# Optimization experiments

Measured on AMD Instinct MI355X. Metric: run time of the kernel, lower is better.

Reference implementation:

```python
import jax, jax.numpy as jnp
import numpy as np

MODEL_DIM = 128
N_FRAMES = 128
N_SAMPLES = 32768
N_TABLES = 8
TABLE_SIZE = 512
BATCH = 8
N_FREQS = 16


def _mlp(x, w1, b1, w2, b2, w3, b3):
    # LinearOutputStack(channels, 3, ...): Linear -> lrelu -> Linear -> lrelu -> Linear
    h = jax.nn.leaky_relu(x @ w1 + b1, 0.2)
    h = jax.nn.leaky_relu(h @ w2 + b2, 0.2)
    return h @ w3 + b3


def _pos_encoded(t, n_freqs=N_FREQS):
    # (t, 1 + 2*n_freqs) = (t, 33): raw position plus sin/cos at geometric freqs
    pos = jnp.linspace(-1.0, 1.0, t, dtype=jnp.float32)
    scales = (2.0 ** jnp.arange(n_freqs, dtype=jnp.float32)) * jnp.pi
    ang = pos[:, None] * scales[None, :]
    return jnp.concatenate([pos[:, None], jnp.sin(ang), jnp.cos(ang)], axis=-1)


def _interp_linear(env, out_size):
    # torch F.interpolate(mode='linear', align_corners=False) from (B, F) to (B, out_size)
    f = env.shape[-1]
    coord = (jnp.arange(out_size, dtype=jnp.float32) + 0.5) * (f / out_size) - 0.5
    i0 = jnp.floor(coord)
    frac = (coord - i0).astype(env.dtype)
    i0c = jnp.clip(i0, 0, f - 1).astype(jnp.int32)
    i1c = jnp.clip(i0 + 1, 0, f - 1).astype(jnp.int32)
    return env[:, i0c] * (1.0 - frac) + env[:, i1c] * frac


def setup_inputs() -> dict:
    key = jax.random.key(0)
    ks = jax.random.split(key, 16)
    wi = 0.02  # weight_init from Experiment
    d = MODEL_DIM

    def lin(k, i, o):
        return jax.random.normal(k, (i, o), jnp.float32) * wi

    inp = {
        "x": jax.random.normal(ks[0], (BATCH, d), jnp.float32),
        "wavetables": jax.random.uniform(ks[1], (N_TABLES, TABLE_SIZE), jnp.float32, -1.0, 1.0),
    }
    specs = {"tc": (d, N_TABLES), "env": (d, N_FRAMES), "pos": (33, d), "sk": (d, TABLE_SIZE)}
    i = 2
    for name, (cin, cout) in specs.items():
        k1, k2, k3 = jax.random.split(ks[i], 3)
        inp[f"{name}_w1"] = lin(k1, cin, d)
        inp[f"{name}_b1"] = jnp.zeros((d,), jnp.float32)
        inp[f"{name}_w2"] = lin(k2, d, d)
        inp[f"{name}_b2"] = jnp.zeros((d,), jnp.float32)
        inp[f"{name}_w3"] = lin(k3, d, cout)
        inp[f"{name}_b3"] = jnp.zeros((cout,), jnp.float32)
        i += 1
    return inp


def reference(x, wavetables,
              tc_w1, tc_b1, tc_w2, tc_b2, tc_w3, tc_b3,
              env_w1, env_b1, env_w2, env_b2, env_w3, env_b3,
              pos_w1, pos_b1, pos_w2, pos_b2, pos_w3, pos_b3,
              sk_w1, sk_b1, sk_w2, sk_b2, sk_w3, sk_b3):
    # table choice: softmax then hard max (straight value * gathered table)
    c = jax.nn.softmax(_mlp(x, tc_w1, tc_b1, tc_w2, tc_b2, tc_w3, tc_b3), axis=-1)
    values = jnp.max(c, axis=-1)          # (B,)
    indices = jnp.argmax(c, axis=-1)      # (B,)

    mx = jnp.max(wavetables, axis=-1, keepdims=True)
    wt = wavetables / (mx + 1e-8)
    sel = wt[indices]                     # (B, TABLE_SIZE)

    env = jnp.abs(_mlp(x, env_w1, env_b1, env_w2, env_b2, env_w3, env_b3))  # (B, N_FRAMES)
    env = _interp_linear(env, N_SAMPLES)  # (B, N_SAMPLES)

    # pos encoding is identical across batch; embed once then broadcast (same math)
    pe = _pos_encoded(N_SAMPLES)          # (T, 33)
    pos = _mlp(pe, pos_w1, pos_b1, pos_w2, pos_b2, pos_w3, pos_b3)  # (T, D)
    pos = pos[None, :, :] + x[:, None, :]  # (B, T, D)

    sk = jax.nn.softmax(_mlp(pos, sk_w1, sk_b1, sk_w2, sk_b2, sk_w3, sk_b3), axis=-1)  # (B, T, K)

    # selected_tables (B,1,K) @ kernel^T (B,K,T) -> (B,1,T)
    sampled = jnp.einsum('bk,btk->bt', sel, sk)
    sampled = sampled * env * values[:, None]
    return sampled[:, None, :]
```

## Files before the change

### kernel.cpp

```cpp
#include <hip/hip_runtime.h>
#include <math.h>

#define D 128
#define B 8
#define T_SAMP 32768
#define K 512
#define NT 8
#define NFRM 128

#define WS_C1   0
#define WS_ENV8 1024
#define WS_SEL  2048
#define WS_VAL  6144
#define WS_B3P  6160
#define WSBF_BYTE 32768
#define OP1 0
#define OP2 9216
#define OP3 26624
#define OS1 44032
#define OS2 61440
#define OS3 78848
#define WTOT 148480
#define WS_NEED (WSBF_BYTE + WTOT*2)

typedef __attribute__((ext_vector_type(8))) short short8;
typedef __attribute__((ext_vector_type(4))) float f32x4;

#define LOG2E 1.4426950408889634f

__device__ __forceinline__ float lrelu(float v){ return fmaxf(v, 0.2f*v); }

__device__ __forceinline__ unsigned cvtpk(float lo, float hi){
    unsigned r;
    asm("v_cvt_pk_bf16_f32 %0, %1, %2" : "=v"(r) : "v"(lo), "v"(hi));
    return r;
}
__device__ __forceinline__ unsigned short bfr(float f){
    unsigned u = __builtin_bit_cast(unsigned, f); u += 0x7fffu + ((u>>16)&1u);
    return (unsigned short)(u>>16);
}
__device__ __forceinline__ float bf2f(short s){
    unsigned u = ((unsigned)(unsigned short)s) << 16;
    return __builtin_bit_cast(float, u);
}
__device__ __forceinline__ float exp2fast(float x){
#if __has_builtin(__builtin_amdgcn_exp2f)
    return __builtin_amdgcn_exp2f(x);
#else
    return __expf(x*0.6931471805599453f);
#endif
}
__device__ __forceinline__ float sin_rev(float fr){
#if __has_builtin(__builtin_amdgcn_sinf)
    return __builtin_amdgcn_sinf(fr);
#else
    return __sinf(fr*6.283185307179586f);
#endif
}
__device__ __forceinline__ float cos_rev(float fr){
#if __has_builtin(__builtin_amdgcn_cosf)
    return __builtin_amdgcn_cosf(fr);
#else
    return __cosf(fr*6.283185307179586f);
#endif
}
__device__ __forceinline__ float pe_val(float pf, int j){
    if (j == 0) return pf;
    if (j > 32) return 0.f;
    const bool is_sin = (j <= 16);
    int e = is_sin ? (j + 125) : (j + 109);
    float sc = __builtin_bit_cast(float, ((unsigned)e) << 23);
    float u = pf * sc;
    float fr = u - floorf(u);
    return is_sin ? sin_rev(fr) : cos_rev(fr);
}

#define VMCNT0 asm volatile("s_waitcnt vmcnt(0)" ::: "memory")

__device__ void layer128(const float* __restrict__ in, const float* __restrict__ w,
                         const float* __restrict__ bias, float* __restrict__ outp,
                         int tid, int mode)
{
    int n = tid & 127, bg = tid >> 7;
    const float* i0 = in + (bg*4+0)*D;
    const float* i1 = in + (bg*4+1)*D;
    const float* i2 = in + (bg*4+2)*D;
    const float* i3 = in + (bg*4+3)*D;
    float bb = bias[n];
    float a0=bb,a1=bb,a2=bb,a3=bb;
    for (int j=0;j<D;j++){
        float wv = w[j*D+n];
        a0 = fmaf(i0[j], wv, a0);
        a1 = fmaf(i1[j], wv, a1);
        a2 = fmaf(i2[j], wv, a2);
        a3 = fmaf(i3[j], wv, a3);
    }
    if (mode==0){ a0=lrelu(a0);a1=lrelu(a1);a2=lrelu(a2);a3=lrelu(a3); }
    else if (mode==1){ a0=fabsf(a0);a1=fabsf(a1);a2=fabsf(a2);a3=fabsf(a3); }
    outp[(bg*4+0)*D+n]=a0;
    outp[(bg*4+1)*D+n]=a1;
    outp[(bg*4+2)*D+n]=a2;
    outp[(bg*4+3)*D+n]=a3;
}

__global__ __launch_bounds__(256) void setup_kernel(
    const float* __restrict__ x, const float* __restrict__ wt,
    const float* __restrict__ tc_w1, const float* __restrict__ tc_b1,
    const float* __restrict__ tc_w2, const float* __restrict__ tc_b2,
    const float* __restrict__ tc_w3, const float* __restrict__ tc_b3,
    const float* __restrict__ env_w1, const float* __restrict__ env_b1,
    const float* __restrict__ env_w2, const float* __restrict__ env_b2,
    const float* __restrict__ env_w3, const float* __restrict__ env_b3,
    const float* __restrict__ sk_w1, const float* __restrict__ sk_b1,
    const float* __restrict__ pos_w1, const float* __restrict__ pos_w2,
    const float* __restrict__ pos_w3, const float* __restrict__ sk_w2,
    const float* __restrict__ sk_w3, const float* __restrict__ sk_b3,
    float* __restrict__ ws)
{
    __shared__ float xl[B*D], buf1[B*D], buf2[B*D];
    __shared__ float lgts[B*NT], pmax[NT*8], mxr[NT];
    __shared__ int idxl[B];
    int tid = threadIdx.x;

    if (blockIdx.x != 0){
        int idx = (blockIdx.x - 1)*256 + tid;
        if (idx >= WTOT) return;
        unsigned short* wb = (unsigned short*)((char*)ws + WSBF_BYTE);
        float v;
        if (idx < OP2){
            int n = idx/72, k = idx%72;
            v = (k < 33) ? pos_w1[k*D + n] : 0.f;
        } else if (idx < OS3){
            int r = idx - OP2; int wsel = r/17408; int i = r%17408;
            int n = i/136, k = i%136;
            const float* W = wsel==0?pos_w2: wsel==1?pos_w3: wsel==2? sk_w1 : sk_w2;
            v = (k < 128) ? W[k*D + n] : 0.f;
        } else {
            int i = idx - OS3; int n = i/136, k = i%136;
            v = (k < 128) ? sk_w3[k*K + n] : 0.f;
        }
        wb[idx] = bfr(v);
        return;
    }

    for (int i=tid;i<B*D;i+=256) xl[i]=x[i];
    for (int i=tid;i<K;i+=256) ws[WS_B3P+i] = sk_b3[i]*LOG2E;
    __syncthreads();
    layer128(xl, tc_w1, tc_b1, buf1, tid, 0);
    __syncthreads();
    layer128(buf1, tc_w2, tc_b2, buf2, tid, 0);
    __syncthreads();
    if (tid < 64){
        int b = tid>>3, n = tid&7;
        float a = tc_b3[n];
        for (int j=0;j<D;j++) a = fmaf(buf2[b*D+j], tc_w3[j*NT+n], a);
        lgts[b*NT+n] = a;
    } else if (tid < 128){
        int r = (tid-64)>>3, p = tid&7;
        float m = -1e30f;
        for (int k=p*64;k<p*64+64;k++) m = fmaxf(m, wt[r*K+k]);
        pmax[r*8+p] = m;
    }
    __syncthreads();
    if (tid < 8){
        int b = tid; float m = -1e30f; int idx = 0;
        for (int n=0;n<NT;n++){ float v = lgts[b*NT+n]; if (v > m){ m=v; idx=n; } }
        float S = 0.f;
        for (int n=0;n<NT;n++) S += expf(lgts[b*NT+n]-m);
        ws[WS_VAL+b] = 1.0f/S;
        idxl[b] = idx;
    } else if (tid < 16){
        int r = tid-8; float m = -1e30f;
        for (int p=0;p<8;p++) m = fmaxf(m, pmax[r*8+p]);
        mxr[r] = m;
    }
    __syncthreads();
    for (int o=tid;o<B*K;o+=256){
        int b = o>>9, k = o&(K-1);
        int id = idxl[b];
        ws[WS_SEL+o] = wt[id*K+k] / (mxr[id] + 1e-8f);
    }
    layer128(xl, env_w1, env_b1, buf1, tid, 0);
    __syncthreads();
    layer128(buf1, env_w2, env_b2, buf2, tid, 0);
    __syncthreads();
    layer128(buf2, env_w3, env_b3, ws+WS_ENV8, tid, 1);
    layer128(xl, sk_w1, sk_b1, ws+WS_C1, tid, 2);
}

template<int NKT, int KSTR, bool ACT>
__device__ __forceinline__ void layerG(const unsigned char* Wp, const unsigned char* inb,
                                       unsigned char* outb, const float* biasp,
                                       int wv, int lg, int lc)
{
    const f32x4 z = {0.f,0.f,0.f,0.f};
    short8 aw[NKT];
    #pragma unroll
    for (int kt=0;kt<NKT;kt++)
        aw[kt] = *(const short8*)(Wp + ((16*wv+lc)*KSTR + 32*kt + 8*lg)*2);
    f32x4 bb = z;
    if (biasp) bb = *(const f32x4*)(biasp + 16*wv + 4*lg);
    #pragma unroll
    for (int rt=0;rt<2;rt++){
        f32x4 d = z;
        #pragma unroll
        for (int kt=0;kt<NKT;kt++){
            short8 bf = *(const short8*)(inb + ((16*rt+lc)*KSTR + 32*kt + 8*lg)*2);
            d = __builtin_amdgcn_mfma_f32_16x16x32_bf16(aw[kt], bf, d, 0,0,0);
        }
        float o0 = d[0]+bb[0], o1 = d[1]+bb[1], o2 = d[2]+bb[2], o3 = d[3]+bb[3];
        if (ACT){ o0=lrelu(o0); o1=lrelu(o1); o2=lrelu(o2); o3=lrelu(o3); }
        uint2 u; u.x = cvtpk(o0,o1); u.y = cvtpk(o2,o3);
        *(uint2*)(outb + ((16*rt+lc)*136 + 16*wv + 4*lg)*2) = u;
    }
}

__global__ __launch_bounds__(512, 4) void synth3(
    const float* __restrict__ pos_b1, const float* __restrict__ pos_b2,
    const float* __restrict__ pos_b3, const float* __restrict__ sk_b2,
    const float* __restrict__ ws, float* __restrict__ out)
{
    __shared__ __align__(16) unsigned char lds[52224];
    unsigned char* WREG_ = lds;
    unsigned char* abA   = lds + 34816;
    unsigned char* abB   = lds + 43520;
    unsigned char* PEb   = abB;

    const int tid = threadIdx.x;
    const int wv = tid >> 6, lane = tid & 63, lg = lane >> 4, lc = lane & 15;
    const int t0 = blockIdx.x * 32;
    const unsigned char* wg = (const unsigned char*)ws + WSBF_BYTE;
    const f32x4 z = {0.f,0.f,0.f,0.f};

    auto stage = [&](int elemoff, unsigned char* dst, int nchunks){
        const unsigned char* src = wg + (size_t)elemoff*2;
        for (int c = wv; c < nchunks; c += 8)
            __builtin_amdgcn_global_load_lds(
                (const __attribute__((address_space(1))) unsigned int*)(src + (c<<10) + lane*16),
                (__attribute__((address_space(3))) unsigned int*)(dst + (c<<10)), 16, 0, 0);
    };

    stage(OP1, WREG_, 18);
    for (int i = tid; i < 1152; i += 512){
        int r = i/36, j0 = (i - r*36)*2;
        float pf = (float)(-1.0 + 2.0*(double)(t0+r)/32767.0);
        float v0 = pe_val(pf, j0);
        float v1 = pe_val(pf, j0+1);
        *(unsigned*)(PEb + (r*72 + j0)*2) = cvtpk(v0, v1);
    }
    VMCNT0; __syncthreads();

    layerG<2,72,true>(WREG_, PEb, abA, pos_b1, wv, lg, lc);
    __syncthreads();
    stage(OP2, WREG_, 34); VMCNT0; __syncthreads();
    layerG<4,136,true>(WREG_, abA, abB, pos_b2, wv, lg, lc);
    __syncthreads();
    stage(OP3, WREG_, 34); VMCNT0; __syncthreads();
    layerG<4,136,false>(WREG_, abB, abA, pos_b3, wv, lg, lc);
    __syncthreads();
    stage(OS1, WREG_, 34); VMCNT0; __syncthreads();
    layerG<4,136,false>(WREG_, abA, abB, nullptr, wv, lg, lc);
    __syncthreads();

    stage(OS2, WREG_, 34);
    short8 hf[2][4];
    {
        const int b = lc & 7;
        const float* c1g = ws + WS_C1 + b*128;
        #pragma unroll
        for (int rtl=0;rtl<2;rtl++){
            int tl = 4*wv + 2*rtl + (lc>>3);
            #pragma unroll
            for (int kt=0;kt<4;kt++){
                short8 a1v = *(const short8*)(abB + (tl*136 + 32*kt + 8*lg)*2);
                const float* cp = c1g + 32*kt + 8*lg;
                f32x4 c0 = *(const f32x4*)cp;
                f32x4 c1v = *(const f32x4*)(cp+4);
                float h[8];
                #pragma unroll
                for (int e=0;e<4;e++){
                    h[e]   = lrelu(bf2f(a1v[e])   + c0[e]);
                    h[4+e] = lrelu(bf2f(a1v[4+e]) + c1v[e]);
                }
                uint4 t4; t4.x=cvtpk(h[0],h[1]); t4.y=cvtpk(h[2],h[3]);
                t4.z=cvtpk(h[4],h[5]); t4.w=cvtpk(h[6],h[7]);
                hf[rtl][kt] = __builtin_bit_cast(short8, t4);
            }
        }
    }
    VMCNT0; __syncthreads();

    short8 h2B[2][4];
    {
        const int sA = (2*(lg&1))*16 + lc;
        const int sB = sA + 16;
        const bool hi = (lg>>1) != 0;
        #pragma unroll
        for (int kt2=0; kt2<4; kt2++){
            unsigned dpk[2][2][2];
            #pragma unroll
            for (int p=0;p<2;p++){
                int n2t = 2*kt2+p;
                short8 aw[4];
                #pragma unroll
                for (int kt=0;kt<4;kt++)
                    aw[kt] = *(const short8*)(WREG_ + ((16*n2t+lc)*136 + 32*kt + 8*lg)*2);
                f32x4 b2 = *(const f32x4*)(sk_b2 + 16*n2t + 4*lg);
                #pragma unroll
                for (int rtl=0;rtl<2;rtl++){
                    f32x4 d = z;
                    #pragma unroll
                    for (int kt=0;kt<4;kt++)
                        d = __builtin_amdgcn_mfma_f32_16x16x32_bf16(aw[kt], hf[rtl][kt], d, 0,0,0);
                    float o0=lrelu(d[0]+b2[0]), o1=lrelu(d[1]+b2[1]);
                    float o2=lrelu(d[2]+b2[2]), o3=lrelu(d[3]+b2[3]);
                    dpk[p][rtl][0] = cvtpk(o0,o1);
                    dpk[p][rtl][1] = cvtpk(o2,o3);
                }
            }
            #pragma unroll
            for (int rtl=0;rtl<2;rtl++){
                unsigned a0 = (unsigned)__shfl((int)dpk[0][rtl][0], sA, 64);
                unsigned b0 = (unsigned)__shfl((int)dpk[1][rtl][0], sA, 64);
                unsigned a1 = (unsigned)__shfl((int)dpk[0][rtl][1], sA, 64);
                unsigned b1 = (unsigned)__shfl((int)dpk[1][rtl][1], sA, 64);
                unsigned a2 = (unsigned)__shfl((int)dpk[0][rtl][0], sB, 64);
                unsigned b2u= (unsigned)__shfl((int)dpk[1][rtl][0], sB, 64);
                unsigned a3 = (unsigned)__shfl((int)dpk[0][rtl][1], sB, 64);
                unsigned b3u= (unsigned)__shfl((int)dpk[1][rtl][1], sB, 64);
                uint4 uu;
                uu.x = hi ? b0 : a0;  uu.y = hi ? b1 : a1;
                uu.z = hi ? b2u : a2; uu.w = hi ? b3u : a3;
                h2B[rtl][kt2] = __builtin_bit_cast(short8, uu);
            }
        }
    }
    __syncthreads();

    float SSa[2][4], WWa[2][4];
    #pragma unroll
    for (int r=0;r<2;r++)
        #pragma unroll
        for (int q=0;q<4;q++){ SSa[r][q]=0.f; WWa[r][q]=0.f; }

    stage(OS3, WREG_, 17); VMCNT0; __syncthreads();
    const float* selg = ws + WS_SEL + (lc & 7)*512;
    const float* b3g  = ws + WS_B3P;
    for (int c=0;c<8;c++){
        const unsigned char* slot = WREG_ + (c&1)*17408;
        if (c < 7) stage(OS3 + (c+1)*8704, WREG_ + ((c+1)&1)*17408, 17);
        #pragma unroll
        for (int nl=0;nl<4;nl++){
            int n3t = 4*c + nl;
            short8 bw[4];
            #pragma unroll
            for (int kt=0;kt<4;kt++)
                bw[kt] = *(const short8*)(slot + ((16*nl+lc)*136 + 32*kt + 8*lg)*2);
            f32x4 d3[2]; d3[0]=z; d3[1]=z;
            #pragma unroll
            for (int rtl=0;rtl<2;rtl++){
                #pragma unroll
                for (int kt=0;kt<4;kt++)
                    d3[rtl] = __builtin_amdgcn_mfma_f32_16x16x32_bf16(bw[kt], h2B[rtl][kt], d3[rtl], 0,0,0);
            }
            f32x4 b3 = *(const f32x4*)(b3g + 16*n3t + 4*lg);
            f32x4 sv = *(const f32x4*)(selg + 16*n3t + 4*lg);
            #pragma unroll
            for (int rtl=0;rtl<2;rtl++){
                #pragma unroll
                for (int q=0;q<4;q++){
                    float e = exp2fast(fmaf(d3[rtl][q], LOG2E, b3[q]));
                    SSa[rtl][q] += e;
                    WWa[rtl][q] = fmaf(e, sv[q], WWa[rtl][q]);
                }
            }
        }
        VMCNT0; __syncthreads();
    }

    #pragma unroll
    for (int rtl=0;rtl<2;rtl++){
        float s = SSa[rtl][0]+SSa[rtl][1]+SSa[rtl][2]+SSa[rtl][3];
        float w = WWa[rtl][0]+WWa[rtl][1]+WWa[rtl][2]+WWa[rtl][3];
        s += __shfl_xor(s, 16, 64); s += __shfl_xor(s, 32, 64);
        w += __shfl_xor(w, 16, 64); w += __shfl_xor(w, 32, 64);
        if (lg == 0){
            int tl = 4*wv + 2*rtl + (lc>>3);
            int b  = lc & 7;
            int t  = t0 + tl;
            float coord = (t + 0.5f)*(1.0f/256.0f) - 0.5f;
            float fi = floorf(coord); float frac = coord - fi;
            int i0 = (int)fi; int i1 = i0 + 1;
            i0 = min(max(i0,0),NFRM-1); i1 = min(max(i1,0),NFRM-1);
            float e0 = ws[WS_ENV8 + b*NFRM + i0], e1 = ws[WS_ENV8 + b*NFRM + i1];
            float envv = e0*(1.0f-frac) + e1*frac;
            out[b*T_SAMP + t] = (w/s) * envv * ws[WS_VAL+b];
        }
    }
}

extern "C" void kernel_launch(void* const* d_in, const int* in_sizes, int n_in,
                              void* d_out, int out_size, void* d_ws, size_t ws_size,
                              hipStream_t stream)
{
    (void)in_sizes; (void)n_in; (void)out_size;
    const float* x       = (const float*)d_in[0];
    const float* wt      = (const float*)d_in[1];
    const float* tc_w1   = (const float*)d_in[2];
    const float* tc_b1   = (const float*)d_in[3];
    const float* tc_w2   = (const float*)d_in[4];
    const float* tc_b2   = (const float*)d_in[5];
    const float* tc_w3   = (const float*)d_in[6];
    const float* tc_b3   = (const float*)d_in[7];
    const float* env_w1  = (const float*)d_in[8];
    const float* env_b1  = (const float*)d_in[9];
    const float* env_w2  = (const float*)d_in[10];
    const float* env_b2  = (const float*)d_in[11];
    const float* env_w3  = (const float*)d_in[12];
    const float* env_b3  = (const float*)d_in[13];
    const float* pos_w1  = (const float*)d_in[14];
    const float* pos_b1  = (const float*)d_in[15];
    const float* pos_w2  = (const float*)d_in[16];
    const float* pos_b2  = (const float*)d_in[17];
    const float* pos_w3  = (const float*)d_in[18];
    const float* pos_b3  = (const float*)d_in[19];
    const float* sk_w1   = (const float*)d_in[20];
    const float* sk_b1   = (const float*)d_in[21];
    const float* sk_w2   = (const float*)d_in[22];
    const float* sk_b2   = (const float*)d_in[23];
    const float* sk_w3   = (const float*)d_in[24];
    const float* sk_b3   = (const float*)d_in[25];
    float* ws  = (float*)d_ws;
    float* out = (float*)d_out;

    if (ws_size < (size_t)WS_NEED) return;

    hipLaunchKernelGGL(setup_kernel, dim3(1 + (WTOT+255)/256), dim3(256), 0, stream,
        x, wt, tc_w1, tc_b1, tc_w2, tc_b2, tc_w3, tc_b3,
        env_w1, env_b1, env_w2, env_b2, env_w3, env_b3,
        sk_w1, sk_b1, pos_w1, pos_w2, pos_w3, sk_w2, sk_w3, sk_b3, ws);

    hipLaunchKernelGGL(synth3, dim3(T_SAMP/32), dim3(512), 0, stream,
        pos_b1, pos_b2, pos_b3, sk_b2, ws, out);
}
```

Baseline: 102.4 us.

## Split positional MLP into separate large-tile kernel writing activations to workspace

Moves the pos-encoding MLP layers and the first sk layer into a new kernel that processes 128 timesteps per block with double-buffered weight staging. Each weight load is amortised over four times more rows. The intermediate bf16 activations (about 9 MB) go through global memory, and the synthesis kernel reads them back. This adds a kernel launch, extra global traffic, and a 157 KB LDS footprint that allows only one block per CU.

New measurement: 109.3 us. +6.8%, slower.

```diff
diff --git a/kernel.cpp b/kernel.cpp
--- a/kernel.cpp
+++ b/kernel.cpp
@@ -22,6 +22,8 @@
 #define OS3 78848
 #define WTOT 148480
 #define WS_NEED (WSBF_BYTE + WTOT*2)
+#define A1_BYTE 335872
+#define WS_NEED2 (A1_BYTE + 32768*272 + 1024)
 
 typedef __attribute__((ext_vector_type(8))) short short8;
 typedef __attribute__((ext_vector_type(4))) float f32x4;
@@ -188,47 +190,21 @@
     layer128(xl, sk_w1, sk_b1, ws+WS_C1, tid, 2);
 }
 
-template<int NKT, int KSTR, bool ACT>
-__device__ __forceinline__ void layerG(const unsigned char* Wp, const unsigned char* inb,
-                                       unsigned char* outb, const float* biasp,
-                                       int wv, int lg, int lc)
+__global__ __launch_bounds__(512, 1) void posk(
+    const float* __restrict__ pos_b1, const float* __restrict__ pos_b2,
+    const float* __restrict__ pos_b3,
+    float* __restrict__ ws)
 {
-    const f32x4 z = {0.f,0.f,0.f,0.f};
-    short8 aw[NKT];
-    #pragma unroll
-    for (int kt=0;kt<NKT;kt++)
-        aw[kt] = *(const short8*)(Wp + ((16*wv+lc)*KSTR + 32*kt + 8*lg)*2);
-    f32x4 bb = z;
-    if (biasp) bb = *(const f32x4*)(biasp + 16*wv + 4*lg);
-    #pragma unroll
-    for (int rt=0;rt<2;rt++){
-        f32x4 d = z;
-        #pragma unroll
-        for (int kt=0;kt<NKT;kt++){
-            short8 bf = *(const short8*)(inb + ((16*rt+lc)*KSTR + 32*kt + 8*lg)*2);
-            d = __builtin_amdgcn_mfma_f32_16x16x32_bf16(aw[kt], bf, d, 0,0,0);
-        }
-        float o0 = d[0]+bb[0], o1 = d[1]+bb[1], o2 = d[2]+bb[2], o3 = d[3]+bb[3];
-        if (ACT){ o0=lrelu(o0); o1=lrelu(o1); o2=lrelu(o2); o3=lrelu(o3); }
-        uint2 u; u.x = cvtpk(o0,o1); u.y = cvtpk(o2,o3);
-        *(uint2*)(outb + ((16*rt+lc)*136 + 16*wv + 4*lg)*2) = u;
-    }
-}
-
-__global__ __launch_bounds__(512, 4) void synth3(
-    const float* __restrict__ pos_b1, const float* __restrict__ pos_b2,
-    const float* __restrict__ pos_b3, const float* __restrict__ sk_b2,
-    const float* __restrict__ ws, float* __restrict__ out)
-{
-    __shared__ __align__(16) unsigned char lds[52224];
-    unsigned char* WREG_ = lds;
-    unsigned char* abA   = lds + 34816;
-    unsigned char* abB   = lds + 43520;
-    unsigned char* PEb   = abB;
+    __shared__ __align__(16) unsigned char lds[157696];
+    unsigned char* Wa  = lds;
+    unsigned char* Wb  = lds + 34816;
+    unsigned char* PE  = lds + 69632;
+    unsigned char* A0  = lds + 88064;
+    unsigned char* A1b = lds + 122880;
 
     const int tid = threadIdx.x;
     const int wv = tid >> 6, lane = tid & 63, lg = lane >> 4, lc = lane & 15;
-    const int t0 = blockIdx.x * 32;
+    const int t0 = blockIdx.x * 128;
     const unsigned char* wg = (const unsigned char*)ws + WSBF_BYTE;
     const f32x4 z = {0.f,0.f,0.f,0.f};
 
@@ -240,29 +216,103 @@
                 (__attribute__((address_space(3))) unsigned int*)(dst + (c<<10)), 16, 0, 0);
     };
 
-    stage(OP1, WREG_, 18);
-    for (int i = tid; i < 1152; i += 512){
-        int r = i/36, j0 = (i - r*36)*2;
+    stage(OP1, Wa, 18);
+    for (int p = tid; p < 4608; p += 512){
+        int r = p/36, j0 = (p - r*36)*2;
         float pf = (float)(-1.0 + 2.0*(double)(t0+r)/32767.0);
         float v0 = pe_val(pf, j0);
         float v1 = pe_val(pf, j0+1);
-        *(unsigned*)(PEb + (r*72 + j0)*2) = cvtpk(v0, v1);
+        *(unsigned*)(PE + r*144 + j0*2) = cvtpk(v0, v1);
     }
     VMCNT0; __syncthreads();
 
-    layerG<2,72,true>(WREG_, PEb, abA, pos_b1, wv, lg, lc);
-    __syncthreads();
-    stage(OP2, WREG_, 34); VMCNT0; __syncthreads();
-    layerG<4,136,true>(WREG_, abA, abB, pos_b2, wv, lg, lc);
-    __syncthreads();
-    stage(OP3, WREG_, 34); VMCNT0; __syncthreads();
-    layerG<4,136,false>(WREG_, abB, abA, pos_b3, wv, lg, lc);
-    __syncthreads();
-    stage(OS1, WREG_, 34); VMCNT0; __syncthreads();
-    layerG<4,136,false>(WREG_, abA, abB, nullptr, wv, lg, lc);
-    __syncthreads();
-
-    stage(OS2, WREG_, 34);
+    stage(OP2, Wb, 34);
+    {
+        int nt = wv;
+        short8 aw[2];
+        #pragma unroll
+        for (int kt=0;kt<2;kt++)
+            aw[kt] = *(const short8*)(Wa + (16*nt+lc)*144 + (32*kt + 8*lg)*2);
+        float b1v[4];
+        #pragma unroll
+        for (int q=0;q<4;q++) b1v[q] = pos_b1[16*nt + 4*lg + q];
+        for (int rt=0; rt<8; rt++){
+            f32x4 d = z;
+            #pragma unroll
+            for (int kt=0;kt<2;kt++){
+                short8 pb = *(const short8*)(PE + (16*rt+lc)*144 + (32*kt + 8*lg)*2);
+                d = __builtin_amdgcn_mfma_f32_16x16x32_bf16(aw[kt], pb, d, 0,0,0);
+            }
+            float o[4];
+            #pragma unroll
+            for (int q=0;q<4;q++) o[q] = lrelu(d[q] + b1v[q]);
+            uint2 u; u.x = cvtpk(o[0],o[1]); u.y = cvtpk(o[2],o[3]);
+            *(uint2*)(A0 + (16*rt+lc)*272 + (16*nt + 4*lg)*2) = u;
+        }
+    }
+    VMCNT0; __syncthreads();
+
+    auto layerP = [&](const unsigned char* Wp, const unsigned char* inb, unsigned char* outb,
+                      const float* bias, bool act){
+        int nt = wv;
+        short8 aw[4];
+        #pragma unroll
+        for (int kt=0;kt<4;kt++)
+            aw[kt] = *(const short8*)(Wp + (16*nt+lc)*272 + (32*kt + 8*lg)*2);
+        float bv[4];
+        #pragma unroll
+        for (int q=0;q<4;q++) bv[q] = bias ? bias[16*nt + 4*lg + q] : 0.f;
+        for (int rt=0; rt<8; rt++){
+            f32x4 d = z;
+            #pragma unroll
+            for (int kt=0;kt<4;kt++){
+                short8 bf = *(const short8*)(inb + (16*rt+lc)*272 + (32*kt + 8*lg)*2);
+                d = __builtin_amdgcn_mfma_f32_16x16x32_bf16(aw[kt], bf, d, 0,0,0);
+            }
+            float o[4];
+            #pragma unroll
+            for (int q=0;q<4;q++){
+                float vv = d[q] + bv[q];
+                o[q] = act ? lrelu(vv) : vv;
+            }
+            uint2 u; u.x = cvtpk(o[0],o[1]); u.y = cvtpk(o[2],o[3]);
+            *(uint2*)(outb + (16*rt+lc)*272 + (16*nt + 4*lg)*2) = u;
+        }
+    };
+
+    stage(OP3, Wa, 34); layerP(Wb, A0, A1b, pos_b2, true);   VMCNT0; __syncthreads();
+    stage(OS1, Wb, 34); layerP(Wa, A1b, A0, pos_b3, false);  VMCNT0; __syncthreads();
+    layerP(Wb, A0, A1b, nullptr, false);                     __syncthreads();
+
+    unsigned char* a1out = (unsigned char*)ws + A1_BYTE + (size_t)blockIdx.x*34816;
+    for (int i = tid; i < 2176; i += 512)
+        *(uint4*)(a1out + i*16) = *(const uint4*)(A1b + i*16);
+}
+
+__global__ __launch_bounds__(512, 4) void synth4(
+    const float* __restrict__ sk_b2,
+    const float* __restrict__ ws, float* __restrict__ out)
+{
+    __shared__ __align__(16) unsigned char lds[34816];
+
+    const int tid = threadIdx.x;
+    const int wv = tid >> 6, lane = tid & 63, lg = lane >> 4, lc = lane & 15;
+    const int t0 = blockIdx.x * 32;
+    const unsigned char* wg = (const unsigned char*)ws + WSBF_BYTE;
+    const f32x4 z = {0.f,0.f,0.f,0.f};
+
+    auto stage = [&](int elemoff, unsigned char* dst, int nchunks){
+        const unsigned char* src = wg + (size_t)elemoff*2;
+        for (int c = wv; c < nchunks; c += 8)
+            __builtin_amdgcn_global_load_lds(
+                (const __attribute__((address_space(1))) unsigned int*)(src + (c<<10) + lane*16),
+                (__attribute__((address_space(3))) unsigned int*)(dst + (c<<10)), 16, 0, 0);
+    };
+
+    stage(OS2, lds, 34);
+
+    const unsigned char* a1g = (const unsigned char*)ws + A1_BYTE
+                             + (size_t)(t0 >> 7)*34816 + (size_t)(t0 & 127)*272;
     short8 hf[2][4];
     {
         const int b = lc & 7;
@@ -272,7 +322,7 @@
             int tl = 4*wv + 2*rtl + (lc>>3);
             #pragma unroll
             for (int kt=0;kt<4;kt++){
-                short8 a1v = *(const short8*)(abB + (tl*136 + 32*kt + 8*lg)*2);
+                short8 a1v = *(const short8*)(a1g + tl*272 + (32*kt + 8*lg)*2);
                 const float* cp = c1g + 32*kt + 8*lg;
                 f32x4 c0 = *(const f32x4*)cp;
                 f32x4 c1v = *(const f32x4*)(cp+4);
@@ -304,7 +354,7 @@
                 short8 aw[4];
                 #pragma unroll
                 for (int kt=0;kt<4;kt++)
-                    aw[kt] = *(const short8*)(WREG_ + ((16*n2t+lc)*136 + 32*kt + 8*lg)*2);
+                    aw[kt] = *(const short8*)(lds + ((16*n2t+lc)*136 + 32*kt + 8*lg)*2);
                 f32x4 b2 = *(const f32x4*)(sk_b2 + 16*n2t + 4*lg);
                 #pragma unroll
                 for (int rtl=0;rtl<2;rtl++){
@@ -343,12 +393,12 @@
         #pragma unroll
         for (int q=0;q<4;q++){ SSa[r][q]=0.f; WWa[r][q]=0.f; }
 
-    stage(OS3, WREG_, 17); VMCNT0; __syncthreads();
+    stage(OS3, lds, 17); VMCNT0; __syncthreads();
     const float* selg = ws + WS_SEL + (lc & 7)*512;
     const float* b3g  = ws + WS_B3P;
     for (int c=0;c<8;c++){
-        const unsigned char* slot = WREG_ + (c&1)*17408;
-        if (c < 7) stage(OS3 + (c+1)*8704, WREG_ + ((c+1)&1)*17408, 17);
+        const unsigned char* slot = lds + (c&1)*17408;
+        if (c < 7) stage(OS3 + (c+1)*8704, lds + ((c+1)&1)*17408, 17);
         #pragma unroll
         for (int nl=0;nl<4;nl++){
             int n3t = 4*c + nl;
@@ -433,13 +483,16 @@
     float* ws  = (float*)d_ws;
     float* out = (float*)d_out;
 
-    if (ws_size < (size_t)WS_NEED) return;
+    if (ws_size < (size_t)WS_NEED2) return;
 
     hipLaunchKernelGGL(setup_kernel, dim3(1 + (WTOT+255)/256), dim3(256), 0, stream,
         x, wt, tc_w1, tc_b1, tc_w2, tc_b2, tc_w3, tc_b3,
         env_w1, env_b1, env_w2, env_b2, env_w3, env_b3,
         sk_w1, sk_b1, pos_w1, pos_w2, pos_w3, sk_w2, sk_w3, sk_b3, ws);
 
-    hipLaunchKernelGGL(synth3, dim3(T_SAMP/32), dim3(512), 0, stream,
-        pos_b1, pos_b2, pos_b3, sk_b2, ws, out);
-}
+    hipLaunchKernelGGL(posk, dim3(T_SAMP/128), dim3(512), 0, stream,
+        pos_b1, pos_b2, pos_b3, ws);
+
+    hipLaunchKernelGGL(synth4, dim3(T_SAMP/32), dim3(512), 0, stream,
+        sk_b2, ws, out);
+}
```

## Read MLP weights directly from global memory instead of staging through LDS

Applied to the files above, without the earlier changes.

Most weight matrices (pos layers, sk layer 1, and the large sk layer 3) are now loaded straight from global memory into MFMA operand registers, which drops the LDS staging, the double buffer and the per-chunk barriers in the final loop. Only sk layer 2 is still staged into LDS. LDS use shrinks from about 52KB to 34KB, which may let more blocks share a CU. The cost is that every wave reads weights through the cache hierarchy, and global-load latency is exposed inside the MFMA loops with no explicit prefetch.

Result: slower. 126.7 us (+23.7%).

```diff
diff --git a/kernel.cpp b/kernel.cpp
--- a/kernel.cpp
+++ b/kernel.cpp
@@ -189,15 +189,15 @@
 }
 
 template<int NKT, int KSTR, bool ACT>
-__device__ __forceinline__ void layerG(const unsigned char* Wp, const unsigned char* inb,
-                                       unsigned char* outb, const float* biasp,
-                                       int wv, int lg, int lc)
+__device__ __forceinline__ void layerGg(const unsigned short* __restrict__ Wg,
+                                        const unsigned char* inb, unsigned char* outb,
+                                        const float* biasp, int wv, int lg, int lc)
 {
     const f32x4 z = {0.f,0.f,0.f,0.f};
     short8 aw[NKT];
     #pragma unroll
     for (int kt=0;kt<NKT;kt++)
-        aw[kt] = *(const short8*)(Wp + ((16*wv+lc)*KSTR + 32*kt + 8*lg)*2);
+        aw[kt] = *(const short8*)(Wg + (16*wv+lc)*KSTR + 32*kt + 8*lg);
     f32x4 bb = z;
     if (biasp) bb = *(const f32x4*)(biasp + 16*wv + 4*lg);
     #pragma unroll
@@ -215,32 +215,22 @@
     }
 }
 
-__global__ __launch_bounds__(512, 4) void synth3(
+__global__ __launch_bounds__(512, 4) void synth5(
     const float* __restrict__ pos_b1, const float* __restrict__ pos_b2,
     const float* __restrict__ pos_b3, const float* __restrict__ sk_b2,
     const float* __restrict__ ws, float* __restrict__ out)
 {
-    __shared__ __align__(16) unsigned char lds[52224];
-    unsigned char* WREG_ = lds;
-    unsigned char* abA   = lds + 34816;
-    unsigned char* abB   = lds + 43520;
-    unsigned char* PEb   = abB;
+    __shared__ __align__(16) unsigned char lds[34816];
+    unsigned char* abA = lds;
+    unsigned char* abB = lds + 8704;
+    unsigned char* PEb = abB;
 
     const int tid = threadIdx.x;
     const int wv = tid >> 6, lane = tid & 63, lg = lane >> 4, lc = lane & 15;
     const int t0 = blockIdx.x * 32;
-    const unsigned char* wg = (const unsigned char*)ws + WSBF_BYTE;
+    const unsigned short* wg16 = (const unsigned short*)((const char*)ws + WSBF_BYTE);
     const f32x4 z = {0.f,0.f,0.f,0.f};
 
-    auto stage = [&](int elemoff, unsigned char* dst, int nchunks){
-        const unsigned char* src = wg + (size_t)elemoff*2;
-        for (int c = wv; c < nchunks; c += 8)
-            __builtin_amdgcn_global_load_lds(
-                (const __attribute__((address_space(1))) unsigned int*)(src + (c<<10) + lane*16),
-                (__attribute__((address_space(3))) unsigned int*)(dst + (c<<10)), 16, 0, 0);
-    };
-
-    stage(OP1, WREG_, 18);
     for (int i = tid; i < 1152; i += 512){
         int r = i/36, j0 = (i - r*36)*2;
         float pf = (float)(-1.0 + 2.0*(double)(t0+r)/32767.0);
@@ -248,21 +238,17 @@
         float v1 = pe_val(pf, j0+1);
         *(unsigned*)(PEb + (r*72 + j0)*2) = cvtpk(v0, v1);
     }
-    VMCNT0; __syncthreads();
-
-    layerG<2,72,true>(WREG_, PEb, abA, pos_b1, wv, lg, lc);
-    __syncthreads();
-    stage(OP2, WREG_, 34); VMCNT0; __syncthreads();
-    layerG<4,136,true>(WREG_, abA, abB, pos_b2, wv, lg, lc);
-    __syncthreads();
-    stage(OP3, WREG_, 34); VMCNT0; __syncthreads();
-    layerG<4,136,false>(WREG_, abB, abA, pos_b3, wv, lg, lc);
-    __syncthreads();
-    stage(OS1, WREG_, 34); VMCNT0; __syncthreads();
-    layerG<4,136,false>(WREG_, abA, abB, nullptr, wv, lg, lc);
-    __syncthreads();
-
-    stage(OS2, WREG_, 34);
+    __syncthreads();
+
+    layerGg<2,72,true>  (wg16+OP1, PEb, abA, pos_b1, wv, lg, lc);
+    __syncthreads();
+    layerGg<4,136,true> (wg16+OP2, abA, abB, pos_b2, wv, lg, lc);
+    __syncthreads();
+    layerGg<4,136,false>(wg16+OP3, abB, abA, pos_b3, wv, lg, lc);
+    __syncthreads();
+    layerGg<4,136,false>(wg16+OS1, abA, abB, nullptr, wv, lg, lc);
+    __syncthreads();
+
     short8 hf[2][4];
     {
         const int b = lc & 7;
@@ -288,6 +274,15 @@
             }
         }
     }
+    __syncthreads();
+
+    {
+        const unsigned char* src = (const unsigned char*)(wg16 + OS2);
+        for (int c = wv; c < 34; c += 8)
+            __builtin_amdgcn_global_load_lds(
+                (const __attribute__((address_space(1))) unsigned int*)(src + (c<<10) + lane*16),
+                (__attribute__((address_space(3))) unsigned int*)(lds + (c<<10)), 16, 0, 0);
+    }
     VMCNT0; __syncthreads();
 
     short8 h2B[2][4];
@@ -304,7 +299,7 @@
                 short8 aw[4];
                 #pragma unroll
                 for (int kt=0;kt<4;kt++)
-                    aw[kt] = *(const short8*)(WREG_ + ((16*n2t+lc)*136 + 32*kt + 8*lg)*2);
+                    aw[kt] = *(const short8*)(lds + ((16*n2t+lc)*136 + 32*kt + 8*lg)*2);
                 f32x4 b2 = *(const f32x4*)(sk_b2 + 16*n2t + 4*lg);
                 #pragma unroll
                 for (int rtl=0;rtl<2;rtl++){
@@ -335,7 +330,6 @@
             }
         }
     }
-    __syncthreads();
 
     float SSa[2][4], WWa[2][4];
     #pragma unroll
@@ -343,19 +337,18 @@
         #pragma unroll
         for (int q=0;q<4;q++){ SSa[r][q]=0.f; WWa[r][q]=0.f; }
 
-    stage(OS3, WREG_, 17); VMCNT0; __syncthreads();
+    const unsigned short* w3g = wg16 + OS3;
     const float* selg = ws + WS_SEL + (lc & 7)*512;
     const float* b3g  = ws + WS_B3P;
+    #pragma unroll 1
     for (int c=0;c<8;c++){
-        const unsigned char* slot = WREG_ + (c&1)*17408;
-        if (c < 7) stage(OS3 + (c+1)*8704, WREG_ + ((c+1)&1)*17408, 17);
         #pragma unroll
         for (int nl=0;nl<4;nl++){
             int n3t = 4*c + nl;
             short8 bw[4];
             #pragma unroll
             for (int kt=0;kt<4;kt++)
-                bw[kt] = *(const short8*)(slot + ((16*nl+lc)*136 + 32*kt + 8*lg)*2);
+                bw[kt] = *(const short8*)(w3g + (64*c + 16*nl + lc)*136 + 32*kt + 8*lg);
             f32x4 d3[2]; d3[0]=z; d3[1]=z;
             #pragma unroll
             for (int rtl=0;rtl<2;rtl++){
@@ -375,7 +368,6 @@
                 }
             }
         }
-        VMCNT0; __syncthreads();
     }
 
     #pragma unroll
@@ -440,6 +432,6 @@
         env_w1, env_b1, env_w2, env_b2, env_w3, env_b3,
         sk_w1, sk_b1, pos_w1, pos_w2, pos_w3, sk_w2, sk_w3, sk_b3, ws);
 
-    hipLaunchKernelGGL(synth3, dim3(T_SAMP/32), dim3(512), 0, stream,
+    hipLaunchKernelGGL(synth5, dim3(T_SAMP/32), dim3(512), 0, stream,
         pos_b1, pos_b2, pos_b3, sk_b2, ws, out);
 }
```
